# Optimization experiments

Measured on AMD Instinct MI355X. Metric: run time of the kernel, lower is better.

Reference implementation:

```python
import jax, jax.numpy as jnp
import numpy as np

P = 0.5
SCALE_TRUE = 10.0
SCALE_WRONG = -10.0
B, C = 2048, 50257


def setup_inputs() -> dict:
    key = jax.random.key(0)
    k1, k2 = jax.random.split(key)
    output = jax.random.normal(k1, (B, C), dtype=jnp.float32)
    labels = jax.random.randint(k2, (B,), 0, C, dtype=jnp.int64)
    return {"output": output, "labels": labels}


def reference(output, labels):
    b, c = output.shape
    rows = jnp.arange(b)

    # tempOut: positive logits scaled by scale_wrong, else 0
    temp_out = jnp.where(output > 0, output * SCALE_WRONG, jnp.zeros_like(output))

    # tempLabels: filled with scale_wrong; target entry per row set to
    # max(|mean(row)|, |row[label]|) * scale_true
    gathered = output[rows, labels]                     # [B]
    row_val = jnp.maximum(jnp.abs(jnp.mean(output, axis=1)), jnp.abs(gathered)) * SCALE_TRUE
    temp_labels = jnp.full_like(output, SCALE_WRONG).at[rows, labels].set(row_val)

    # L1 loss (mean reduction over all elements)
    l1 = jnp.mean(jnp.abs(temp_out - temp_labels))

    # Cross-entropy (mean over batch)
    log_probs = jax.nn.log_softmax(output, axis=1)      # [B, C]
    ce = -jnp.mean(log_probs[rows, labels])

    return P * l1 + (1.0 - P) * ce
```

## Files before the change

### kernel.cpp

```cpp
#include <hip/hip_runtime.h>
#include <stdint.h>

#define BATCH 2048
#define NCLS  50257
#define LOG2E 1.44269504088896340736f
#define LN2   0.69314718055994530942f

typedef float v4f __attribute__((ext_vector_type(4)));

__device__ __forceinline__ float l1_base(float v) {
    return fabsf(1.f - fmaxf(v, 0.f));
}

template<bool USE_WS>
__global__ __launch_bounds__(256, 4) void custom_loss_kernel(
    const float* __restrict__ x,
    const int*   __restrict__ labels,
    float*       __restrict__ out)
{
    const int row = blockIdx.x;
    const int tid = threadIdx.x;
    const float* rp = x + (size_t)row * NCLS;

    float s0=0.f, s1=0.f, s2=0.f, s3=0.f;
    float a0=0.f, a1=0.f, a2=0.f, a3=0.f;
    float e0=0.f, e1=0.f, e2=0.f, e3=0.f;

    const int peel_full = (int)(((16u - ((uintptr_t)rp & 15u)) & 15u) >> 2);
    const int peel = peel_full > NCLS ? NCLS : peel_full;
    if (tid < peel) {
        float v = rp[tid];
        s0 += v; a0 += l1_base(v); e0 += exp2f(v * LOG2E);
    }

    const v4f* rp4 = (const v4f*)(rp + peel);
    const int n4 = (NCLS - peel) >> 2;
    int i = tid;
    for (; i + 768 < n4; i += 1024) {
        v4f a = rp4[i];
        v4f b = rp4[i + 256];
        v4f c = rp4[i + 512];
        v4f d = rp4[i + 768];

        s0 += (a.x + a.y) + (a.z + a.w);
        s1 += (b.x + b.y) + (b.z + b.w);
        s2 += (c.x + c.y) + (c.z + c.w);
        s3 += (d.x + d.y) + (d.z + d.w);

        a0 += (l1_base(a.x) + l1_base(a.y)) + (l1_base(a.z) + l1_base(a.w));
        a1 += (l1_base(b.x) + l1_base(b.y)) + (l1_base(b.z) + l1_base(b.w));
        a2 += (l1_base(c.x) + l1_base(c.y)) + (l1_base(c.z) + l1_base(c.w));
        a3 += (l1_base(d.x) + l1_base(d.y)) + (l1_base(d.z) + l1_base(d.w));

        e0 += (exp2f(a.x * LOG2E) + exp2f(a.y * LOG2E))
            + (exp2f(a.z * LOG2E) + exp2f(a.w * LOG2E));
        e1 += (exp2f(b.x * LOG2E) + exp2f(b.y * LOG2E))
            + (exp2f(b.z * LOG2E) + exp2f(b.w * LOG2E));
        e2 += (exp2f(c.x * LOG2E) + exp2f(c.y * LOG2E))
            + (exp2f(c.z * LOG2E) + exp2f(c.w * LOG2E));
        e3 += (exp2f(d.x * LOG2E) + exp2f(d.y * LOG2E))
            + (exp2f(d.z * LOG2E) + exp2f(d.w * LOG2E));
    }
    for (; i < n4; i += 256) {
        v4f a = rp4[i];
        s0 += (a.x + a.y) + (a.z + a.w);
        a0 += (l1_base(a.x) + l1_base(a.y)) + (l1_base(a.z) + l1_base(a.w));
        e0 += (exp2f(a.x * LOG2E) + exp2f(a.y * LOG2E))
            + (exp2f(a.z * LOG2E) + exp2f(a.w * LOG2E));
    }

    const int tail = peel + (n4 << 2);
    for (int j = tail + tid; j < NCLS; j += 256) {
        float v = rp[j];
        s0 += v; a0 += l1_base(v); e0 += exp2f(v * LOG2E);
    }

    float S = (s0 + s1) + (s2 + s3);
    float L = (a0 + a1) + (a2 + a3);
    float E = (e0 + e1) + (e2 + e3);

    #pragma unroll
    for (int off = 32; off > 0; off >>= 1) {
        S += __shfl_down(S, off);
        L += __shfl_down(L, off);
        E += __shfl_down(E, off);
    }

    __shared__ float red[3][4];
    const int lane = tid & 63, wave = tid >> 6;
    if (lane == 0) { red[0][wave] = S; red[1][wave] = L; red[2][wave] = E; }
    __syncthreads();

    if (tid == 0) {
        float Sa = (red[0][0] + red[0][1]) + (red[0][2] + red[0][3]);
        float La = (red[1][0] + red[1][1]) + (red[1][2] + red[1][3]);
        float Ea = (red[2][0] + red[2][1]) + (red[2][2] + red[2][3]);

        const int   label = labels[row];
        const float g     = rp[label];

        const float mean    = Sa * (1.f / (float)NCLS);
        const float row_val = fmaxf(fabsf(mean), fabsf(g)) * 10.f;
        const float tout_g  = (g > 0.f) ? -10.f * g : 0.f;
        const float l1_row  = 10.f * La - 10.f * l1_base(g) + fabsf(tout_g - row_val);

        const float ce_row  = __log2f(Ea) * LN2 - g;

        const float inv_bc = 1.f / ((float)BATCH * (float)NCLS);
        const float inv_b  = 1.f / (float)BATCH;
        const float contrib = 0.5f * l1_row * inv_bc + 0.5f * ce_row * inv_b;

        if (USE_WS) out[row] = contrib;
        else        atomicAdd(out, contrib);
    }
}

__global__ __launch_bounds__(1024) void reduce_rows_kernel(
    const float* __restrict__ rc, float* __restrict__ result)
{
    const int tid = threadIdx.x;
    float v = rc[tid] + rc[tid + 1024];
    #pragma unroll
    for (int off = 32; off > 0; off >>= 1) v += __shfl_down(v, off);

    __shared__ float red[16];
    const int lane = tid & 63, wave = tid >> 6;
    if (lane == 0) red[wave] = v;
    __syncthreads();

    if (tid == 0) {
        float t = 0.f;
        #pragma unroll
        for (int w = 0; w < 16; ++w) t += red[w];
        *result = t;
    }
}

extern "C" void kernel_launch(void* const* d_in, const int* in_sizes, int n_in,
                              void* d_out, int out_size, void* d_ws, size_t ws_size,
                              hipStream_t stream) {
    const float* x      = (const float*)d_in[0];
    const int*   labels = (const int*)d_in[1];
    float*       out    = (float*)d_out;

    if (d_ws && ws_size >= BATCH * sizeof(float)) {
        float* rc = (float*)d_ws;
        custom_loss_kernel<true><<<BATCH, 256, 0, stream>>>(x, labels, rc);
        reduce_rows_kernel<<<1, 1024, 0, stream>>>(rc, out);
    } else {
        (void)hipMemsetAsync(out, 0, sizeof(float), stream);
        custom_loss_kernel<false><<<BATCH, 256, 0, stream>>>(x, labels, out);
    }
}
```

Measured before the change: 538.6 us.

## Use nontemporal row loads and atomic accumulation instead of a second reduce kernel

Row loads in the main loops now use nontemporal loads, so streamed logits do not pollute the cache. The separate reduce kernel and workspace path are dropped, and each block atomically adds its contribution after a memset. The occupancy hint on launch bounds is also removed. This trades a second kernel launch for 2048 contended atomics on one address, and makes the float summation order nondeterministic.

```diff
diff --git a/kernel.cpp b/kernel.cpp
--- a/kernel.cpp
+++ b/kernel.cpp
@@ -12,11 +12,10 @@
     return fabsf(1.f - fmaxf(v, 0.f));
 }
 
-template<bool USE_WS>
-__global__ __launch_bounds__(256, 4) void custom_loss_kernel(
+__global__ __launch_bounds__(256) void custom_loss_kernel(
     const float* __restrict__ x,
     const int*   __restrict__ labels,
-    float*       __restrict__ out)
+    float*       __restrict__ result)
 {
     const int row = blockIdx.x;
     const int tid = threadIdx.x;
@@ -37,10 +36,10 @@
     const int n4 = (NCLS - peel) >> 2;
     int i = tid;
     for (; i + 768 < n4; i += 1024) {
-        v4f a = rp4[i];
-        v4f b = rp4[i + 256];
-        v4f c = rp4[i + 512];
-        v4f d = rp4[i + 768];
+        v4f a = __builtin_nontemporal_load(&rp4[i]);
+        v4f b = __builtin_nontemporal_load(&rp4[i + 256]);
+        v4f c = __builtin_nontemporal_load(&rp4[i + 512]);
+        v4f d = __builtin_nontemporal_load(&rp4[i + 768]);
 
         s0 += (a.x + a.y) + (a.z + a.w);
         s1 += (b.x + b.y) + (b.z + b.w);
@@ -62,7 +61,7 @@
             + (exp2f(d.z * LOG2E) + exp2f(d.w * LOG2E));
     }
     for (; i < n4; i += 256) {
-        v4f a = rp4[i];
+        v4f a = __builtin_nontemporal_load(&rp4[i]);
         s0 += (a.x + a.y) + (a.z + a.w);
         a0 += (l1_base(a.x) + l1_base(a.y)) + (l1_base(a.z) + l1_base(a.w));
         e0 += (exp2f(a.x * LOG2E) + exp2f(a.y * LOG2E))
@@ -110,29 +109,7 @@
         const float inv_b  = 1.f / (float)BATCH;
         const float contrib = 0.5f * l1_row * inv_bc + 0.5f * ce_row * inv_b;
 
-        if (USE_WS) out[row] = contrib;
-        else        atomicAdd(out, contrib);
-    }
-}
-
-__global__ __launch_bounds__(1024) void reduce_rows_kernel(
-    const float* __restrict__ rc, float* __restrict__ result)
-{
-    const int tid = threadIdx.x;
-    float v = rc[tid] + rc[tid + 1024];
-    #pragma unroll
-    for (int off = 32; off > 0; off >>= 1) v += __shfl_down(v, off);
-
-    __shared__ float red[16];
-    const int lane = tid & 63, wave = tid >> 6;
-    if (lane == 0) red[wave] = v;
-    __syncthreads();
-
-    if (tid == 0) {
-        float t = 0.f;
-        #pragma unroll
-        for (int w = 0; w < 16; ++w) t += red[w];
-        *result = t;
+        atomicAdd(result, contrib);
     }
 }
 
@@ -143,12 +120,7 @@
     const int*   labels = (const int*)d_in[1];
     float*       out    = (float*)d_out;
 
-    if (d_ws && ws_size >= BATCH * sizeof(float)) {
-        float* rc = (float*)d_ws;
-        custom_loss_kernel<true><<<BATCH, 256, 0, stream>>>(x, labels, rc);
-        reduce_rows_kernel<<<1, 1024, 0, stream>>>(rc, out);
-    } else {
-        (void)hipMemsetAsync(out, 0, sizeof(float), stream);
-        custom_loss_kernel<false><<<BATCH, 256, 0, stream>>>(x, labels, out);
-    }
+    (void)hipMemsetAsync(out, 0, sizeof(float), stream);
+
+    custom_loss_kernel<<<BATCH, 256, 0, stream>>>(x, labels, out);
 }
```

After: 516.6 us. -4.1%, faster.
